# Kernel tuning notes

Measured on AMD Instinct MI355X. Metric: run time of the kernel, lower is better.

Reference implementation:

```python
import jax, jax.numpy as jnp
import numpy as np

NUM_HEADS = 8
HEAD_DIM = 64
LATENT = NUM_HEADS * HEAD_DIM  # 512
IN_CH = 256


def setup_inputs() -> dict:
    key = jax.random.key(0)
    k1, k2, k3, k4 = jax.random.split(key, 4)
    b, c, h, w = 16, IN_CH, 64, 64
    net = jax.random.normal(k1, (b, c, h, w), dtype=jnp.float32)
    # 1x1 conv weights (out_ch, in_ch); scaled like kaiming-ish init
    w_qkv = jax.random.normal(k2, (3 * LATENT, c), dtype=jnp.float32) / np.sqrt(c)
    w_out = jax.random.normal(k3, (c, LATENT), dtype=jnp.float32) / np.sqrt(LATENT)
    b_out = jax.random.normal(k4, (c,), dtype=jnp.float32) * 0.01
    return {"net": net, "w_qkv": w_qkv, "w_out": w_out, "b_out": b_out}


def reference(net, w_qkv, w_out, b_out):
    b, c, h, w = net.shape
    n = h * w
    # 1x1 conv == channel GEMM: (b, 3L, n)
    qkv = jnp.einsum("bchw,oc->bohw", net, w_qkv).reshape(b, 3, NUM_HEADS, HEAD_DIM, n)
    q, k, v = qkv[:, 0], qkv[:, 1], qkv[:, 2]  # each (b, H, D, n)
    k = jax.nn.softmax(k, axis=-1)  # softmax over spatial tokens
    context = jnp.einsum("bhdn,bhen->bhde", k, v)  # (b, H, D, D)
    out = jnp.einsum("bhde,bhdn->bhen", context, q)  # (b, H, D, n)
    out = out.reshape(b, LATENT, h, w)
    # output 1x1 conv with bias
    out = jnp.einsum("blhw,cl->bchw", out, w_out) + b_out[None, :, None, None]
    return out
```

## Files before the change

kernel.cpp:

```cpp
#include <hip/hip_runtime.h>


typedef unsigned short u16;
typedef unsigned int u32;
typedef __attribute__((ext_vector_type(4))) u16 u16x4;
typedef __attribute__((ext_vector_type(4))) u32 u32x4;
typedef __attribute__((ext_vector_type(4))) float f32x4;
typedef __attribute__((ext_vector_type(8))) short bf16x8;

__device__ __forceinline__ u16 f2bf(float f) {
  union { float f; u32 u; } x; x.f = f;
  u32 r = x.u + 0x7fffu + ((x.u >> 16) & 1u);
  return (u16)(r >> 16);
}

__device__ __forceinline__ void async16(const u16* g, u16* l) {
  __builtin_amdgcn_global_load_lds(
      (const __attribute__((address_space(1))) void*)g,
      (__attribute__((address_space(3))) void*)l, 16, 0, 0);
}

__global__ __launch_bounds__(256) void cast_w(const float* __restrict__ w,
                                              u16* __restrict__ o) {
  int i = (blockIdx.x * 256 + threadIdx.x) * 4;
  f32x4 v = *(const f32x4*)(w + i);
  u16x4 u;
  u[0] = f2bf(v[0]); u[1] = f2bf(v[1]); u[2] = f2bf(v[2]); u[3] = f2bf(v[3]);
  *(u16x4*)(o + i) = u;
}

__global__ __launch_bounds__(256) void transpose_cast_g(const float* __restrict__ in,
                                                        u16* __restrict__ out,
                                                        int R, int C) {
  __shared__ float t[64][65];
  const int b = blockIdx.z, r0 = blockIdx.y * 64, c0 = blockIdx.x * 64;
  const float* ip = in + (size_t)b * R * C;
  u16* op = out + (size_t)b * R * C;
  const int tid = threadIdx.x;
  const int col4 = (tid & 15) * 4, rr0 = tid >> 4;
#pragma unroll
  for (int i = 0; i < 4; ++i) {
    int r = rr0 + i * 16;
    f32x4 v = *(const f32x4*)(ip + (size_t)(r0 + r) * C + c0 + col4);
    t[r][col4 + 0] = v[0]; t[r][col4 + 1] = v[1];
    t[r][col4 + 2] = v[2]; t[r][col4 + 3] = v[3];
  }
  __syncthreads();
  const int cc4 = (tid & 15) * 4, nr0 = tid >> 4;
#pragma unroll
  for (int i = 0; i < 4; ++i) {
    int nr = nr0 + i * 16;
    u16x4 u;
    u[0] = f2bf(t[cc4 + 0][nr]); u[1] = f2bf(t[cc4 + 1][nr]);
    u[2] = f2bf(t[cc4 + 2][nr]); u[3] = f2bf(t[cc4 + 3][nr]);
    *(u16x4*)(op + (size_t)(c0 + nr) * R + r0 + cc4) = u;
  }
}

__global__ __launch_bounds__(512, 2) void kv_ctx_fused(
    const u16* __restrict__ wkv,
    const u16* __restrict__ netT,
    float* __restrict__ ctxp,
    float* __restrict__ sump) {
  __shared__ __align__(16) u16 Bs[2][16384];
  __shared__ __align__(16) u16 ekL[4096];
  __shared__ __align__(16) u16 vL[4096];

  const int flat = blockIdx.x;
  const int xcd = flat & 7, inner = flat >> 3;
  const int b = 2 * xcd + (inner >> 5);
  const int h = (inner >> 2) & 7;
  const int s = inner & 3;

  const int tid = threadIdx.x, lane = tid & 63, wid = tid >> 6;
  const int wq = wid & 3, wn = wid >> 2;
  const int lr = lane & 15, lg = lane >> 4;
  const bool isK = (wq < 2);

  bf16x8 af[2][8];
#pragma unroll
  for (int mi = 0; mi < 2; ++mi) {
    const int r = wq * 32 + mi * 16 + lr;
    const int grow = (r < 64) ? h * 64 + r : 512 + h * 64 + (r - 64);
#pragma unroll
    for (int kk = 0; kk < 8; ++kk)
      af[mi][kk] = *(const bf16x8*)(wkv + (size_t)grow * 256 + kk * 32 + lg * 8);
  }

  const u16* Bsrc = netT + ((size_t)b * 4096 + s * 1024) * 256;
  const int srow = tid >> 5;
  const int sslot = tid & 31;
  auto stage = [&](int c, int buf) {
    const u16* src = Bsrc + (size_t)c * 64 * 256;
#pragma unroll
    for (int i = 0; i < 4; ++i) {
      const int row = i * 16 + srow;
      const int scol = ((sslot ^ (row & 7)) * 8);
      async16(src + row * 256 + scol, &Bs[buf][i * 4096 + tid * 8]);
    }
  };

  f32x4 cacc[2] = {};
  f32x4 sacc = {};
  bf16x8 ones8;
#pragma unroll
  for (int j = 0; j < 8; ++j) ((u16*)&ones8)[j] = 0x3F80;

  auto ctx_acc = [&]() {
#pragma unroll
    for (int kk2 = 0; kk2 < 2; ++kk2) {
      const int d = wq * 16 + lr;
      bf16x8 ekf = *(const bf16x8*)&ekL[d * 64 + (((kk2 * 4 + lg) ^ (d & 7)) * 8)];
#pragma unroll
      for (int ei = 0; ei < 2; ++ei) {
        const int e = wn * 32 + ei * 16 + lr;
        bf16x8 vf = *(const bf16x8*)&vL[e * 64 + (((kk2 * 4 + lg) ^ (e & 7)) * 8)];
        cacc[ei] = __builtin_amdgcn_mfma_f32_16x16x32_bf16(ekf, vf, cacc[ei], 0, 0, 0);
      }
      if (wn == 0)
        sacc = __builtin_amdgcn_mfma_f32_16x16x32_bf16(ekf, ones8, sacc, 0, 0, 0);
    }
  };

  stage(0, 0);
  asm volatile("s_waitcnt vmcnt(0)" ::: "memory");
  __syncthreads();

  for (int c = 0; c < 16; ++c) {
    const int buf = c & 1;
    if (c + 1 < 16) {
      stage(c + 1, buf ^ 1);
      asm volatile("s_waitcnt vmcnt(4)" ::: "memory");
    } else {
      asm volatile("s_waitcnt vmcnt(0)" ::: "memory");
    }
    __syncthreads();

    f32x4 kvacc[2][2] = {};
    __builtin_amdgcn_s_setprio(1);
#pragma unroll
    for (int kk = 0; kk < 8; ++kk) {
      bf16x8 bfr[2];
#pragma unroll
      for (int ni = 0; ni < 2; ++ni) {
        const int nrow = wn * 32 + ni * 16 + lr;
        bfr[ni] = *(const bf16x8*)&Bs[buf][nrow * 256 + (((kk * 4 + lg) ^ (nrow & 7)) * 8)];
      }
#pragma unroll
      for (int mi = 0; mi < 2; ++mi)
#pragma unroll
        for (int ni = 0; ni < 2; ++ni)
          kvacc[mi][ni] = __builtin_amdgcn_mfma_f32_16x16x32_bf16(
              af[mi][kk], bfr[ni], kvacc[mi][ni], 0, 0, 0);
    }
    if (c > 0) ctx_acc();
    __builtin_amdgcn_s_setprio(0);
    __syncthreads();

    u16* dstL = isK ? ekL : vL;
#pragma unroll
    for (int mi = 0; mi < 2; ++mi)
#pragma unroll
      for (int ni = 0; ni < 2; ++ni)
#pragma unroll
        for (int j = 0; j < 4; ++j) {
          float v = kvacc[mi][ni][j];
          if (isK) v = __expf(v);
          const u32 u = __float_as_uint(v);
          const u16 bv = (u16)((u + 0x8000u) >> 16);
          const int dd = (wq & 1) * 32 + mi * 16 + lg * 4 + j;
          const int n = wn * 32 + ni * 16 + lr;
          dstL[dd * 64 + (((n >> 3) ^ (dd & 7)) * 8) + (n & 7)] = bv;
        }
  }
  __syncthreads();
  ctx_acc();

  float* cp = ctxp + (((size_t)(b * 8 + h) * 4 + s) * 4096);
#pragma unroll
  for (int ei = 0; ei < 2; ++ei)
#pragma unroll
    for (int j = 0; j < 4; ++j) {
      const int d = wq * 16 + lg * 4 + j;
      const int e = wn * 32 + ei * 16 + lr;
      cp[d * 64 + e] = cacc[ei][j];
    }
  if (wn == 0 && lr == 0) {
#pragma unroll
    for (int j = 0; j < 4; ++j)
      sump[((size_t)(b * 8 + h) * 4 + s) * 64 + wq * 16 + lg * 4 + j] = sacc[j];
  }
}

__global__ __launch_bounds__(256) void fold_w2(const float* __restrict__ ctxp,
                                               const float* __restrict__ sump,
                                               const float* __restrict__ wout,
                                               u16* __restrict__ W2) {
  __shared__ float cl[16 * 64];
  __shared__ float sl[16];
  const int bh = blockIdx.x, dq = blockIdx.y;
  const int b = bh >> 3, h = bh & 7;
  const int tid = threadIdx.x;
  f32x4 v4 = {0.f, 0.f, 0.f, 0.f};
#pragma unroll
  for (int ch = 0; ch < 4; ++ch)
    v4 += *(const f32x4*)(ctxp + ((size_t)bh * 4 + ch) * 4096 + dq * 1024 + tid * 4);
  *(f32x4*)&cl[tid * 4] = v4;
  if (tid < 16) {
    float ss = 0.f;
#pragma unroll
    for (int ch = 0; ch < 4; ++ch)
      ss += sump[((size_t)bh * 4 + ch) * 64 + dq * 16 + tid];
    sl[tid] = ss;
  }
  __syncthreads();
  const int c = tid;
  f32x4 wv[16];
  const float* wrow = wout + (size_t)c * 512 + h * 64;
#pragma unroll
  for (int i = 0; i < 16; ++i) wv[i] = *(const f32x4*)(wrow + i * 4);
#pragma unroll
  for (int d = 0; d < 16; ++d) {
    f32x4 s4 = {0.f, 0.f, 0.f, 0.f};
#pragma unroll
    for (int e4 = 0; e4 < 16; ++e4) {
      f32x4 cv = *(const f32x4*)&cl[d * 64 + e4 * 4];
      s4 += wv[e4] * cv;
    }
    const float s = (s4[0] + s4[1] + s4[2] + s4[3]) / sl[d];
    W2[((size_t)b * 256 + c) * 512 + h * 64 + dq * 16 + d] = f2bf(s);
  }
}

template <int LD, int NK, int MODE>
__global__ __launch_bounds__(256) void gemm128(const u16* __restrict__ A,
                                               const u16* __restrict__ B,
                                               size_t aStride, size_t bStride,
                                               void* __restrict__ O0,
                                               const float* __restrict__ bias) {
  __shared__ __align__(16) u16 SM[32768];
  const int b = blockIdx.z, mt = blockIdx.y, nt = blockIdx.x;
  const int tid = threadIdx.x, lane = tid & 63, wid = tid >> 6;
  const int wr = wid >> 1, wc = wid & 1, lr = lane & 15, lg = lane >> 4;
  const u16* Ap = A + (size_t)b * aStride + (size_t)mt * 128 * LD;
  const u16* Bp = B + (size_t)b * bStride + (size_t)nt * 128 * LD;

  auto stage = [&](int buf, int ks) {
    const int k0 = ks * 64;
#pragma unroll
    for (int i = 0; i < 4; ++i) {
      const int idx = i * 2048 + tid * 8;
      const int r = idx >> 6, c = idx & 63;
      async16(Ap + (size_t)r * LD + k0 + c, SM + buf * 8192 + i * 2048 + wid * 512);
      async16(Bp + (size_t)r * LD + k0 + c, SM + 16384 + buf * 8192 + i * 2048 + wid * 512);
    }
  };

  f32x4 acc[4][4] = {};
  stage(0, 0);
  asm volatile("s_waitcnt vmcnt(0)" ::: "memory");
  __syncthreads();
  for (int ks = 0; ks < NK; ++ks) {
    const int buf = ks & 1;
    if (ks + 1 < NK) stage(buf ^ 1, ks + 1);
    const u16* Ab = SM + buf * 8192;
    const u16* Bb = SM + 16384 + buf * 8192;
#pragma unroll
    for (int kk = 0; kk < 2; ++kk) {
      bf16x8 afm[4], bfr[4];
#pragma unroll
      for (int mi = 0; mi < 4; ++mi)
        afm[mi] = *(const bf16x8*)(Ab + (wr * 64 + mi * 16 + lr) * 64 + kk * 32 + lg * 8);
#pragma unroll
      for (int ni = 0; ni < 4; ++ni)
        bfr[ni] = *(const bf16x8*)(Bb + (wc * 64 + ni * 16 + lr) * 64 + kk * 32 + lg * 8);
#pragma unroll
      for (int mi = 0; mi < 4; ++mi)
#pragma unroll
        for (int ni = 0; ni < 4; ++ni)
          acc[mi][ni] = __builtin_amdgcn_mfma_f32_16x16x32_bf16(afm[mi], bfr[ni], acc[mi][ni], 0, 0, 0);
    }
    asm volatile("s_waitcnt vmcnt(0)" ::: "memory");
    __syncthreads();
  }

  if constexpr (MODE == 2) {
    u16* Cs = SM;
#pragma unroll
    for (int mi = 0; mi < 4; ++mi)
#pragma unroll
      for (int ni = 0; ni < 4; ++ni)
#pragma unroll
        for (int j = 0; j < 4; ++j)
          Cs[(wr * 64 + mi * 16 + lg * 4 + j) * 128 + wc * 64 + ni * 16 + lr] =
              f2bf(acc[mi][ni][j]);
    __syncthreads();
    u16* dst = (u16*)O0;
#pragma unroll
    for (int p = 0; p < 8; ++p) {
      const int idx = p * 2048 + tid * 8;
      const int r = idx >> 7, cc = idx & 127;
      *(u32x4*)(dst + ((size_t)b * 256 + mt * 128 + r) * 256 + nt * 128 + cc) =
          *(const u32x4*)(Cs + idx);
    }
  } else {
    float* Cf = (float*)SM;
#pragma unroll
    for (int mi = 0; mi < 4; ++mi)
#pragma unroll
      for (int ni = 0; ni < 4; ++ni)
#pragma unroll
        for (int j = 0; j < 4; ++j) {
          const int row = wr * 64 + mi * 16 + lg * 4 + j;
          Cf[row * 128 + wc * 64 + ni * 16 + lr] = acc[mi][ni][j] + bias[mt * 128 + row];
        }
    __syncthreads();
    float* op = (float*)O0;
#pragma unroll
    for (int p = 0; p < 16; ++p) {
      const int idx = p * 1024 + tid * 4;
      const int r = idx >> 7, cc = idx & 127;
      *(f32x4*)(op + ((size_t)b * 256 + mt * 128 + r) * 4096 + nt * 128 + cc) =
          *(const f32x4*)(Cf + idx);
    }
  }
}

extern "C" void kernel_launch(void* const* d_in, const int* in_sizes, int n_in,
                              void* d_out, int out_size, void* d_ws, size_t ws_size,
                              hipStream_t stream) {
  const float* net  = (const float*)d_in[0];
  const float* wqkv = (const float*)d_in[1];
  const float* wout = (const float*)d_in[2];
  const float* bout = (const float*)d_in[3];
  float* out = (float*)d_out;

  char* ws = (char*)d_ws;
  u16*   netT = (u16*)(ws + 0);
  float* ctxp = (float*)(ws + 33554432);
  float* sump = (float*)(ws + 41943040);
  u16*   W2   = (u16*)(ws + 42074112);
  u16*   W3   = (u16*)(ws + 46268416);
  u16*   wkv  = (u16*)(ws + 48365568);
  u16*   wqTb = (u16*)(ws + 48889856);

  cast_w<<<256, 256, 0, stream>>>(wqkv + 512 * 256, wkv);
  transpose_cast_g<<<dim3(64, 4, 16), 256, 0, stream>>>(net, netT, 256, 4096);
  transpose_cast_g<<<dim3(4, 8, 1), 256, 0, stream>>>(wqkv, wqTb, 512, 256);
  kv_ctx_fused<<<512, 512, 0, stream>>>(wkv, netT, ctxp, sump);
  fold_w2<<<dim3(128, 4), 256, 0, stream>>>(ctxp, sump, wout, W2);
  gemm128<512, 8, 2><<<dim3(2, 2, 16), 256, 0, stream>>>(
      W2, wqTb, (size_t)256 * 512, 0, W3, nullptr);
  gemm128<256, 4, 1><<<dim3(32, 2, 16), 256, 0, stream>>>(
      W3, netT, (size_t)256 * 256, (size_t)4096 * 256, out, bout);
}
```

Before: 132.1 us.

## Load B fragments directly from global, double-buffer ek/v LDS, remap blocks

Drops the async global-to-LDS staging of the activation tile. Each wave now reads its bf16 B fragments straight from global memory into registers, which removes the large Bs buffer and one barrier per chunk. The ek/v LDS tiles are double-buffered so the context MFMA for the previous chunk can run before the current projection. The block-to-(b,h,s) mapping changes so that the 8 heads sharing the same activation slice land on the same XCD, where they can reuse it through L2. Smaller LDS allows the launch bound to rise to 4 blocks per CU, at the risk of exposed global-load latency since there is no explicit prefetch.

```diff
diff --git a/kernel.cpp b/kernel.cpp
--- a/kernel.cpp
+++ b/kernel.cpp
@@ -57,20 +57,19 @@
   }
 }
 
-__global__ __launch_bounds__(512, 2) void kv_ctx_fused(
+__global__ __launch_bounds__(512, 4) void kv_ctx_fused(
     const u16* __restrict__ wkv,
     const u16* __restrict__ netT,
     float* __restrict__ ctxp,
     float* __restrict__ sump) {
-  __shared__ __align__(16) u16 Bs[2][16384];
-  __shared__ __align__(16) u16 ekL[4096];
-  __shared__ __align__(16) u16 vL[4096];
-
-  const int flat = blockIdx.x;
-  const int xcd = flat & 7, inner = flat >> 3;
-  const int b = 2 * xcd + (inner >> 5);
-  const int h = (inner >> 2) & 7;
-  const int s = inner & 3;
+  __shared__ __align__(16) u16 ekL[2][4096];
+  __shared__ __align__(16) u16 vL[2][4096];
+
+  const int orig = blockIdx.x;
+  const int xcd = orig & 7, ix = orig >> 3;
+  const int g = xcd * 8 + (ix >> 3);
+  const int h = ix & 7;
+  const int b = g >> 2, s = g & 3;
 
   const int tid = threadIdx.x, lane = tid & 63, wid = tid >> 6;
   const int wq = wid & 3, wn = wid >> 2;
@@ -87,18 +86,8 @@
       af[mi][kk] = *(const bf16x8*)(wkv + (size_t)grow * 256 + kk * 32 + lg * 8);
   }
 
-  const u16* Bsrc = netT + ((size_t)b * 4096 + s * 1024) * 256;
-  const int srow = tid >> 5;
-  const int sslot = tid & 31;
-  auto stage = [&](int c, int buf) {
-    const u16* src = Bsrc + (size_t)c * 64 * 256;
-#pragma unroll
-    for (int i = 0; i < 4; ++i) {
-      const int row = i * 16 + srow;
-      const int scol = ((sslot ^ (row & 7)) * 8);
-      async16(src + row * 256 + scol, &Bs[buf][i * 4096 + tid * 8]);
-    }
-  };
+  const u16* brow0 = netT + ((size_t)b * 4096 + s * 1024 + wn * 32 + lr) * 256 + lg * 8;
+  const u16* brow1 = brow0 + 16 * 256;
 
   f32x4 cacc[2] = {};
   f32x4 sacc = {};
@@ -106,15 +95,15 @@
 #pragma unroll
   for (int j = 0; j < 8; ++j) ((u16*)&ones8)[j] = 0x3F80;
 
-  auto ctx_acc = [&]() {
+  auto ctx_acc = [&](int p) {
 #pragma unroll
     for (int kk2 = 0; kk2 < 2; ++kk2) {
       const int d = wq * 16 + lr;
-      bf16x8 ekf = *(const bf16x8*)&ekL[d * 64 + (((kk2 * 4 + lg) ^ (d & 7)) * 8)];
+      bf16x8 ekf = *(const bf16x8*)&ekL[p][d * 64 + (((kk2 * 4 + lg) ^ (d & 7)) * 8)];
 #pragma unroll
       for (int ei = 0; ei < 2; ++ei) {
         const int e = wn * 32 + ei * 16 + lr;
-        bf16x8 vf = *(const bf16x8*)&vL[e * 64 + (((kk2 * 4 + lg) ^ (e & 7)) * 8)];
+        bf16x8 vf = *(const bf16x8*)&vL[p][e * 64 + (((kk2 * 4 + lg) ^ (e & 7)) * 8)];
         cacc[ei] = __builtin_amdgcn_mfma_f32_16x16x32_bf16(ekf, vf, cacc[ei], 0, 0, 0);
       }
       if (wn == 0)
@@ -122,42 +111,26 @@
     }
   };
 
-  stage(0, 0);
-  asm volatile("s_waitcnt vmcnt(0)" ::: "memory");
-  __syncthreads();
-
   for (int c = 0; c < 16; ++c) {
-    const int buf = c & 1;
-    if (c + 1 < 16) {
-      stage(c + 1, buf ^ 1);
-      asm volatile("s_waitcnt vmcnt(4)" ::: "memory");
-    } else {
-      asm volatile("s_waitcnt vmcnt(0)" ::: "memory");
-    }
-    __syncthreads();
+    const int p = c & 1;
 
     f32x4 kvacc[2][2] = {};
     __builtin_amdgcn_s_setprio(1);
+    if (c > 0) ctx_acc(p ^ 1);
 #pragma unroll
     for (int kk = 0; kk < 8; ++kk) {
-      bf16x8 bfr[2];
-#pragma unroll
-      for (int ni = 0; ni < 2; ++ni) {
-        const int nrow = wn * 32 + ni * 16 + lr;
-        bfr[ni] = *(const bf16x8*)&Bs[buf][nrow * 256 + (((kk * 4 + lg) ^ (nrow & 7)) * 8)];
+      bf16x8 b0 = *(const bf16x8*)(brow0 + kk * 32);
+      bf16x8 b1 = *(const bf16x8*)(brow1 + kk * 32);
+#pragma unroll
+      for (int mi = 0; mi < 2; ++mi) {
+        kvacc[mi][0] = __builtin_amdgcn_mfma_f32_16x16x32_bf16(af[mi][kk], b0, kvacc[mi][0], 0, 0, 0);
+        kvacc[mi][1] = __builtin_amdgcn_mfma_f32_16x16x32_bf16(af[mi][kk], b1, kvacc[mi][1], 0, 0, 0);
       }
-#pragma unroll
-      for (int mi = 0; mi < 2; ++mi)
-#pragma unroll
-        for (int ni = 0; ni < 2; ++ni)
-          kvacc[mi][ni] = __builtin_amdgcn_mfma_f32_16x16x32_bf16(
-              af[mi][kk], bfr[ni], kvacc[mi][ni], 0, 0, 0);
-    }
-    if (c > 0) ctx_acc();
+    }
     __builtin_amdgcn_s_setprio(0);
-    __syncthreads();
-
-    u16* dstL = isK ? ekL : vL;
+    brow0 += 64 * 256; brow1 += 64 * 256;
+
+    u16* dstL = isK ? ekL[p] : vL[p];
 #pragma unroll
     for (int mi = 0; mi < 2; ++mi)
 #pragma unroll
@@ -172,9 +145,9 @@
           const int n = wn * 32 + ni * 16 + lr;
           dstL[dd * 64 + (((n >> 3) ^ (dd & 7)) * 8) + (n & 7)] = bv;
         }
-  }
-  __syncthreads();
-  ctx_acc();
+    __syncthreads();
+  }
+  ctx_acc(1);
 
   float* cp = ctxp + (((size_t)(b * 8 + h) * 4 + s) * 4096);
 #pragma unroll
```

Result: slower. 207.6 us (+57.2%).

## Halve token chunk in fused kv/context kernel to raise occupancy

Applied to the files above, without the earlier changes.

Shrinks the per-iteration token chunk from 64 to 32 rows, halving the shared-memory staging, exp(K) and V buffers, and raises launch bounds to allow four blocks per CU. The loop now runs 32 iterations with half the MFMAs each, and the context accumulation for the previous chunk is moved ahead of the new projection MFMAs. The aim is more resident waves to hide load latency. The cost is twice as many barriers and pipeline steps per block and tighter register limits, which could cause spills.

```diff
diff --git a/kernel.cpp b/kernel.cpp
--- a/kernel.cpp
+++ b/kernel.cpp
@@ -57,14 +57,14 @@
   }
 }
 
-__global__ __launch_bounds__(512, 2) void kv_ctx_fused(
+__global__ __launch_bounds__(512, 4) void kv_ctx_fused(
     const u16* __restrict__ wkv,
     const u16* __restrict__ netT,
     float* __restrict__ ctxp,
     float* __restrict__ sump) {
-  __shared__ __align__(16) u16 Bs[2][16384];
-  __shared__ __align__(16) u16 ekL[4096];
-  __shared__ __align__(16) u16 vL[4096];
+  __shared__ __align__(16) u16 Bs[2][8192];
+  __shared__ __align__(16) u16 ekL[2048];
+  __shared__ __align__(16) u16 vL[2048];
 
   const int flat = blockIdx.x;
   const int xcd = flat & 7, inner = flat >> 3;
@@ -91,9 +91,9 @@
   const int srow = tid >> 5;
   const int sslot = tid & 31;
   auto stage = [&](int c, int buf) {
-    const u16* src = Bsrc + (size_t)c * 64 * 256;
-#pragma unroll
-    for (int i = 0; i < 4; ++i) {
+    const u16* src = Bsrc + (size_t)c * 32 * 256;
+#pragma unroll
+    for (int i = 0; i < 2; ++i) {
       const int row = i * 16 + srow;
       const int scol = ((sslot ^ (row & 7)) * 8);
       async16(src + row * 256 + scol, &Bs[buf][i * 4096 + tid * 8]);
@@ -107,71 +107,58 @@
   for (int j = 0; j < 8; ++j) ((u16*)&ones8)[j] = 0x3F80;
 
   auto ctx_acc = [&]() {
-#pragma unroll
-    for (int kk2 = 0; kk2 < 2; ++kk2) {
-      const int d = wq * 16 + lr;
-      bf16x8 ekf = *(const bf16x8*)&ekL[d * 64 + (((kk2 * 4 + lg) ^ (d & 7)) * 8)];
-#pragma unroll
-      for (int ei = 0; ei < 2; ++ei) {
-        const int e = wn * 32 + ei * 16 + lr;
-        bf16x8 vf = *(const bf16x8*)&vL[e * 64 + (((kk2 * 4 + lg) ^ (e & 7)) * 8)];
-        cacc[ei] = __builtin_amdgcn_mfma_f32_16x16x32_bf16(ekf, vf, cacc[ei], 0, 0, 0);
-      }
-      if (wn == 0)
-        sacc = __builtin_amdgcn_mfma_f32_16x16x32_bf16(ekf, ones8, sacc, 0, 0, 0);
-    }
+    const int d = wq * 16 + lr;
+    bf16x8 ekf = *(const bf16x8*)&ekL[d * 32 + ((lg ^ (d & 3)) * 8)];
+#pragma unroll
+    for (int ei = 0; ei < 2; ++ei) {
+      const int e = wn * 32 + ei * 16 + lr;
+      bf16x8 vf = *(const bf16x8*)&vL[e * 32 + ((lg ^ (e & 3)) * 8)];
+      cacc[ei] = __builtin_amdgcn_mfma_f32_16x16x32_bf16(ekf, vf, cacc[ei], 0, 0, 0);
+    }
+    if (wn == 0)
+      sacc = __builtin_amdgcn_mfma_f32_16x16x32_bf16(ekf, ones8, sacc, 0, 0, 0);
   };
 
   stage(0, 0);
   asm volatile("s_waitcnt vmcnt(0)" ::: "memory");
   __syncthreads();
 
-  for (int c = 0; c < 16; ++c) {
-    const int buf = c & 1;
-    if (c + 1 < 16) {
-      stage(c + 1, buf ^ 1);
-      asm volatile("s_waitcnt vmcnt(4)" ::: "memory");
+  for (int c = 0; c < 32; ++c) {
+    const int p = c & 1;
+    if (c + 1 < 32) {
+      stage(c + 1, p ^ 1);
+      asm volatile("s_waitcnt vmcnt(2)" ::: "memory");
     } else {
       asm volatile("s_waitcnt vmcnt(0)" ::: "memory");
     }
     __syncthreads();
 
-    f32x4 kvacc[2][2] = {};
+    f32x4 kvacc[2] = {};
     __builtin_amdgcn_s_setprio(1);
+    if (c > 0) ctx_acc();
+    const int nrow = wn * 16 + lr;
 #pragma unroll
     for (int kk = 0; kk < 8; ++kk) {
-      bf16x8 bfr[2];
-#pragma unroll
-      for (int ni = 0; ni < 2; ++ni) {
-        const int nrow = wn * 32 + ni * 16 + lr;
-        bfr[ni] = *(const bf16x8*)&Bs[buf][nrow * 256 + (((kk * 4 + lg) ^ (nrow & 7)) * 8)];
+      bf16x8 bfr = *(const bf16x8*)&Bs[p][nrow * 256 + (((kk * 4 + lg) ^ (nrow & 7)) * 8)];
+      kvacc[0] = __builtin_amdgcn_mfma_f32_16x16x32_bf16(af[0][kk], bfr, kvacc[0], 0, 0, 0);
+      kvacc[1] = __builtin_amdgcn_mfma_f32_16x16x32_bf16(af[1][kk], bfr, kvacc[1], 0, 0, 0);
+    }
+    __builtin_amdgcn_s_setprio(0);
+    __syncthreads();
+
+    u16* dstL = isK ? ekL : vL;
+#pragma unroll
+    for (int mi = 0; mi < 2; ++mi)
+#pragma unroll
+      for (int j = 0; j < 4; ++j) {
+        float v = kvacc[mi][j];
+        if (isK) v = __expf(v);
+        const u32 u = __float_as_uint(v);
+        const u16 bv = (u16)((u + 0x8000u) >> 16);
+        const int dd = (wq & 1) * 32 + mi * 16 + lg * 4 + j;
+        const int n = wn * 16 + lr;
+        dstL[dd * 32 + (((n >> 3) ^ (dd & 3)) * 8) + (n & 7)] = bv;
       }
-#pragma unroll
-      for (int mi = 0; mi < 2; ++mi)
-#pragma unroll
-        for (int ni = 0; ni < 2; ++ni)
-          kvacc[mi][ni] = __builtin_amdgcn_mfma_f32_16x16x32_bf16(
-              af[mi][kk], bfr[ni], kvacc[mi][ni], 0, 0, 0);
-    }
-    if (c > 0) ctx_acc();
-    __builtin_amdgcn_s_setprio(0);
-    __syncthreads();
-
-    u16* dstL = isK ? ekL : vL;
-#pragma unroll
-    for (int mi = 0; mi < 2; ++mi)
-#pragma unroll
-      for (int ni = 0; ni < 2; ++ni)
-#pragma unroll
-        for (int j = 0; j < 4; ++j) {
-          float v = kvacc[mi][ni][j];
-          if (isK) v = __expf(v);
-          const u32 u = __float_as_uint(v);
-          const u16 bv = (u16)((u + 0x8000u) >> 16);
-          const int dd = (wq & 1) * 32 + mi * 16 + lg * 4 + j;
-          const int n = wn * 32 + ni * 16 + lr;
-          dstL[dd * 64 + (((n >> 3) ^ (dd & 7)) * 8) + (n & 7)] = bv;
-        }
   }
   __syncthreads();
   ctx_acc();
```

Result: faster. 117.1 us (-11.3%).
